# Optimization experiments

Measured on AMD Instinct MI355X. Metric: run time of the kernel, lower is better.

## Reference

```python
import jax, jax.numpy as jnp
import numpy as np

VOCAB, D_IN, D_H, D_OUT = 32000, 512, 1024, 32000
B, S = 64, 512

def setup_inputs() -> dict:
    key = jax.random.key(0)
    ks = jax.random.split(key, 6)
    xav = lambda k, shp: jax.random.uniform(k, shp, jnp.float32, -1.0, 1.0) * np.sqrt(6.0 / (shp[0] + shp[1]))
    return {
        "tokens": jax.random.randint(ks[0], (B, S), 0, VOCAB),
        "h0": jnp.zeros((B, D_H), jnp.float32),
        "embed_table": jax.random.normal(ks[1], (VOCAB, D_IN), jnp.float32),
        "W_ih": xav(ks[2], (D_IN, D_H)),
        "W_hh": xav(ks[3], (D_H, D_H)),
        "bias_hh": jnp.zeros((D_H,), jnp.float32),
        "W_out": xav(ks[4], (D_H, D_OUT)),
        "b_out": jnp.zeros((D_OUT,), jnp.float32),
    }

def reference(tokens, h0, embed_table, W_ih, W_hh, bias_hh, W_out, b_out):
    # embed: [B,S,D_in] -> seq-first [S,B,D_in]
    x = embed_table[tokens].transpose(1, 0, 2)
    # precompute input projection for all timesteps (one big GEMM)
    xw = jnp.einsum("sbi,ih->sbh", x, W_ih) + bias_hh

    def step(h, xw_t):
        h_new = jnp.tanh(xw_t + h @ W_hh)
        return h_new, None

    h_last, _ = jax.lax.scan(step, h0, xw)
    y_pred = h_last @ W_out + b_out  # [B, D_OUT]
    return y_pred
```

## Files before the change

### kernel.cpp

```cpp
#include <hip/hip_runtime.h>

#define D_IN 512
#define D_H 1024
#define D_OUT 32000
#define NB 64
#define NS 512

typedef __attribute__((ext_vector_type(8))) short short8;
typedef __attribute__((ext_vector_type(8))) __bf16 bf16x8;
typedef __attribute__((ext_vector_type(4))) float f32x4;

__device__ __forceinline__ unsigned short f2bf(float f) {
  unsigned int u = __float_as_uint(f);
  u += 0x7fffu + ((u >> 16) & 1u);
  return (unsigned short)(u >> 16);
}
__device__ __forceinline__ float bf2f(unsigned short s) {
  return __uint_as_float(((unsigned int)s) << 16);
}

__device__ __forceinline__ f32x4 mfma_bf16(short8 a, short8 b, f32x4 c) {
  return __builtin_amdgcn_mfma_f32_16x16x32_bf16(
      __builtin_bit_cast(bf16x8, a), __builtin_bit_cast(bf16x8, b), c, 0, 0, 0);
}

union HQ { unsigned long long q[2]; short8 s; };

__global__ __launch_bounds__(256) void rnn_init(const float* __restrict__ h0,
                                                unsigned short* __restrict__ hex,
                                                unsigned int* __restrict__ flags) {
  int idx = blockIdx.x * 256 + threadIdx.x;
  int bg = idx >> 10;
  int k = idx & 1023;
  int g = bg >> 4, bl = bg & 15;
  float v = h0[idx];
  unsigned short hh = f2bf(v);
  unsigned short hl = f2bf(v - bf2f(hh));
  size_t base = ((size_t)(g * 2 + 0) * 2) * 16384 + (size_t)bl * 1024 + k;
  hex[base] = hh;
  hex[base + 16384] = hl;
  if (blockIdx.x == 0) flags[threadIdx.x] = 0u;
}

__global__ __launch_bounds__(256) void rnn_pack_wih(const float* __restrict__ W_ih,
                                                    unsigned short* __restrict__ bhi,
                                                    unsigned short* __restrict__ blo) {
  int idx = blockIdx.x * 256 + threadIdx.x;
  int j = idx & 7;
  int l = (idx >> 3) & 63;
  int kc = (idx >> 9) & 15;
  int nc = idx >> 13;
  int k = kc * 32 + ((l >> 4) << 3) + j;
  int n = nc * 16 + (l & 15);
  float v = W_ih[(size_t)k * D_H + n];
  unsigned short h = f2bf(v);
  bhi[idx] = h;
  blo[idx] = f2bf(v - bf2f(h));
}

__global__ __launch_bounds__(256) void rnn_stage1(const int* __restrict__ tokens,
                                                  const float* __restrict__ embed,
                                                  const unsigned short* __restrict__ bhi,
                                                  const unsigned short* __restrict__ blo,
                                                  const float* __restrict__ bias,
                                                  float* __restrict__ xw) {
  int bx = blockIdx.x;
  int mt = bx >> 4, nt = bx & 15;
  int tid = threadIdx.x;
  int w = tid >> 6, l = tid & 63;
  int q = l >> 4;

  int m = mt * 64 + w * 16 + (l & 15);
  int b = m & 63, t = m >> 6;
  int tok = tokens[b * NS + t];
  const float* arow = embed + (size_t)tok * D_IN;

  f32x4 acc[4];
#pragma unroll
  for (int i = 0; i < 4; ++i) acc[i] = (f32x4){0.f, 0.f, 0.f, 0.f};

  for (int c = 0; c < 16; ++c) {
    const float* ap = arow + c * 32 + q * 8;
    float4 f0 = *(const float4*)ap;
    float4 f1 = *(const float4*)(ap + 4);
    float fa[8] = {f0.x, f0.y, f0.z, f0.w, f1.x, f1.y, f1.z, f1.w};
    short8 ahi, alo;
#pragma unroll
    for (int j = 0; j < 8; ++j) {
      unsigned short hh = f2bf(fa[j]);
      ahi[j] = (short)hh;
      alo[j] = (short)f2bf(fa[j] - bf2f(hh));
    }
#pragma unroll
    for (int ni = 0; ni < 4; ++ni) {
      int ncg = nt * 4 + ni;
      size_t boff = ((size_t)(ncg * 16 + c) * 64 + l) * 8;
      short8 bh = *(const short8*)(bhi + boff);
      short8 bl_ = *(const short8*)(blo + boff);
      acc[ni] = mfma_bf16(ahi, bh, acc[ni]);
      acc[ni] = mfma_bf16(alo, bh, acc[ni]);
      acc[ni] = mfma_bf16(ahi, bl_, acc[ni]);
    }
  }

#pragma unroll
  for (int ni = 0; ni < 4; ++ni) {
    int col = nt * 64 + ni * 16 + (l & 15);
    float bv = bias[col];
#pragma unroll
    for (int r = 0; r < 4; ++r) {
      int row = mt * 64 + w * 16 + q * 4 + r;
      xw[(size_t)row * D_H + col] = acc[ni][r] + bv;
    }
  }
}

__global__ __launch_bounds__(256, 1) void rnn_recur(const float* __restrict__ xw,
                                                    const float* __restrict__ W_hh,
                                                    unsigned short* __restrict__ hex,
                                                    unsigned int* __restrict__ flags,
                                                    float* __restrict__ h_last) {
  __shared__ short Whi[32768];
  __shared__ short Wlo[32768];
  __shared__ float red[4][16][33];

  const int tid = threadIdx.x;
  const int bx = blockIdx.x;
  const int g = bx >> 5;
  const int jt = bx & 31;
  const int jcol0 = jt * 32;
  const int w = tid >> 6;
  const int l = tid & 63;
  const int q = l >> 4;
  const int b_lane = l & 15;

  for (int v = tid; v < 32768; v += 256) {
    int j = v & 7;
    int ll = (v >> 3) & 63;
    int c = (v >> 9) & 31;
    int s = v >> 14;
    int k = c * 32 + ((ll >> 4) << 3) + j;
    int n = s * 16 + (ll & 15);
    float wv = W_hh[(size_t)k * D_H + jcol0 + n];
    unsigned short hh = f2bf(wv);
    Whi[v] = (short)hh;
    Wlo[v] = (short)f2bf(wv - bf2f(hh));
  }
  __syncthreads();

  unsigned int* flg = flags + g * 32;

  const int be = tid >> 4;
  const int je2 = (tid & 15) * 2;
  const int brow = g * 16 + be;

  for (int t = 1; t <= NS; ++t) {
    const float* xwp = xw + ((size_t)(t - 1) * 64 + brow) * D_H + jcol0 + je2;
    float xv0 = xwp[0];
    float xv1 = xwp[1];

    if (tid < 64) {
      unsigned int target = (unsigned int)(t - 1);
      while (1) {
        unsigned int v = __hip_atomic_load(&flg[l & 31], __ATOMIC_RELAXED,
                                           __HIP_MEMORY_SCOPE_AGENT);
        if (__all((int)(v >= target))) break;
      }
    }
    __syncthreads();

    int rbuf = (t - 1) & 1;
    const unsigned long long* hhi =
        (const unsigned long long*)(hex + ((size_t)(g * 2 + rbuf) * 2 + 0) * 16384);
    const unsigned long long* hlo =
        (const unsigned long long*)(hex + ((size_t)(g * 2 + rbuf) * 2 + 1) * 16384);

    HQ ha[8], hl_[8];
#pragma unroll
    for (int i = 0; i < 8; ++i) {
      int c = w * 8 + i;
      int k = c * 32 + q * 8;
      size_t qi = ((size_t)b_lane * 1024 + k) >> 2;
      ha[i].q[0] = __hip_atomic_load(hhi + qi, __ATOMIC_RELAXED, __HIP_MEMORY_SCOPE_AGENT);
      ha[i].q[1] = __hip_atomic_load(hhi + qi + 1, __ATOMIC_RELAXED, __HIP_MEMORY_SCOPE_AGENT);
      hl_[i].q[0] = __hip_atomic_load(hlo + qi, __ATOMIC_RELAXED, __HIP_MEMORY_SCOPE_AGENT);
      hl_[i].q[1] = __hip_atomic_load(hlo + qi + 1, __ATOMIC_RELAXED, __HIP_MEMORY_SCOPE_AGENT);
    }

    f32x4 a00 = {0.f, 0.f, 0.f, 0.f}, a01 = a00, a02 = a00;
    f32x4 a10 = a00, a11 = a00, a12 = a00;
#pragma unroll
    for (int i = 0; i < 8; ++i) {
      int c = w * 8 + i;
      short8 bh0 = *(const short8*)(Whi + c * 512 + l * 8);
      short8 bl0 = *(const short8*)(Wlo + c * 512 + l * 8);
      short8 bh1 = *(const short8*)(Whi + 16384 + c * 512 + l * 8);
      short8 bl1 = *(const short8*)(Wlo + 16384 + c * 512 + l * 8);
      a00 = mfma_bf16(ha[i].s, bh0, a00);
      a01 = mfma_bf16(hl_[i].s, bh0, a01);
      a02 = mfma_bf16(ha[i].s, bl0, a02);
      a10 = mfma_bf16(ha[i].s, bh1, a10);
      a11 = mfma_bf16(hl_[i].s, bh1, a11);
      a12 = mfma_bf16(ha[i].s, bl1, a12);
    }
    f32x4 s0 = a00 + a01 + a02;
    f32x4 s1 = a10 + a11 + a12;
#pragma unroll
    for (int r = 0; r < 4; ++r) {
      red[w][q * 4 + r][b_lane] = s0[r];
      red[w][q * 4 + r][16 + b_lane] = s1[r];
    }
    __syncthreads();

    float z0 = red[0][be][je2] + red[1][be][je2] + red[2][be][je2] +
               red[3][be][je2] + xv0;
    float z1 = red[0][be][je2 + 1] + red[1][be][je2 + 1] + red[2][be][je2 + 1] +
               red[3][be][je2 + 1] + xv1;
    float hv0 = tanhf(z0);
    float hv1 = tanhf(z1);
    unsigned short h0h = f2bf(hv0), h1h = f2bf(hv1);
    unsigned short h0l = f2bf(hv0 - bf2f(h0h)), h1l = f2bf(hv1 - bf2f(h1h));
    int wbuf = t & 1;
    size_t obase = (size_t)be * 1024 + jcol0 + je2;
    unsigned int* dhi =
        (unsigned int*)(hex + ((size_t)(g * 2 + wbuf) * 2 + 0) * 16384 + obase);
    unsigned int* dlo =
        (unsigned int*)(hex + ((size_t)(g * 2 + wbuf) * 2 + 1) * 16384 + obase);
    unsigned int phi = (unsigned int)h0h | ((unsigned int)h1h << 16);
    unsigned int plo = (unsigned int)h0l | ((unsigned int)h1l << 16);
    __hip_atomic_store(dhi, phi, __ATOMIC_RELAXED, __HIP_MEMORY_SCOPE_AGENT);
    __hip_atomic_store(dlo, plo, __ATOMIC_RELAXED, __HIP_MEMORY_SCOPE_AGENT);
    if (t == NS) {
      h_last[(size_t)brow * 1024 + jcol0 + je2] = hv0;
      h_last[(size_t)brow * 1024 + jcol0 + je2 + 1] = hv1;
    }

    asm volatile("s_waitcnt vmcnt(0)" ::: "memory");
    __syncthreads();
    if (tid == 0)
      __hip_atomic_store(&flg[jt], (unsigned int)t, __ATOMIC_RELAXED,
                         __HIP_MEMORY_SCOPE_AGENT);
  }
}

__global__ __launch_bounds__(256, 2) void rnn_out(const float* __restrict__ h_last,
                                                  const float* __restrict__ W_out,
                                                  const float* __restrict__ b_out,
                                                  float* __restrict__ out) {
  __shared__ float smem[16384];
  int tid = threadIdx.x;
  int jl = tid & 127;
  int kh = tid >> 7;
  int j = blockIdx.x * 128 + jl;

  float acc[64];
#pragma unroll
  for (int b = 0; b < 64; ++b) acc[b] = 0.f;

  for (int kc = 0; kc < 4; ++kc) {
    __syncthreads();
    for (int v = tid; v < 16384; v += 256) {
      int kh2 = v >> 13;
      int b = (v >> 7) & 63;
      int kk = v & 127;
      smem[v] = h_last[(size_t)b * 1024 + kh2 * 512 + kc * 128 + kk];
    }
    __syncthreads();
    int kbase = kh * 512 + kc * 128;
    for (int kkc = 0; kkc < 16; ++kkc) {
      float wreg[8];
#pragma unroll
      for (int i = 0; i < 8; ++i)
        wreg[i] = W_out[(size_t)(kbase + kkc * 8 + i) * D_OUT + j];
#pragma unroll
      for (int b = 0; b < 64; ++b) {
        const float* hp = &smem[kh * 8192 + b * 128 + kkc * 8];
#pragma unroll
        for (int i = 0; i < 8; ++i) acc[b] += hp[i] * wreg[i];
      }
    }
  }
  __syncthreads();
  if (kh == 1) {
#pragma unroll
    for (int b = 0; b < 64; ++b) smem[jl * 65 + b] = acc[b];
  }
  __syncthreads();
  if (kh == 0) {
    float bo = b_out[j];
#pragma unroll
    for (int b = 0; b < 64; ++b)
      out[(size_t)b * D_OUT + j] = acc[b] + smem[jl * 65 + b] + bo;
  }
}

extern "C" void kernel_launch(void* const* d_in, const int* in_sizes, int n_in,
                              void* d_out, int out_size, void* d_ws, size_t ws_size,
                              hipStream_t stream) {
  const int* tokens = (const int*)d_in[0];
  const float* h0 = (const float*)d_in[1];
  const float* embed = (const float*)d_in[2];
  const float* W_ih = (const float*)d_in[3];
  const float* W_hh = (const float*)d_in[4];
  const float* bias_hh = (const float*)d_in[5];
  const float* W_out = (const float*)d_in[6];
  const float* b_out = (const float*)d_in[7];
  float* out = (float*)d_out;

  char* ws = (char*)d_ws;
  float* xw = (float*)(ws);
  unsigned short* wih_hi = (unsigned short*)(ws + 134217728);
  unsigned short* wih_lo = (unsigned short*)(ws + 135266304);
  unsigned short* hex = (unsigned short*)(ws + 136314880);
  unsigned int* flags = (unsigned int*)(ws + 136839168);
  float* h_last = (float*)(ws + 136840192);

  rnn_init<<<256, 256, 0, stream>>>(h0, hex, flags);
  rnn_pack_wih<<<2048, 256, 0, stream>>>(W_ih, wih_hi, wih_lo);
  rnn_stage1<<<8192, 256, 0, stream>>>(tokens, embed, wih_hi, wih_lo, bias_hh, xw);
  rnn_recur<<<128, 256, 0, stream>>>(xw, W_hh, hex, flags, h_last);
  rnn_out<<<250, 256, 0, stream>>>(h_last, W_out, b_out, out);
}
```

Measured before the change: 3.600 ms.

## Replace flag barrier with tagged hidden-state words for flagless cross-block sync

Removes the per-step flag array and its store-wait-barrier-flag handshake in the recurrent kernel. Each hidden-state element pair is now packed as a 64-bit word (hi and lo bf16 parts) with a parity tag in the low bit of the lo parts. Readers spin on the data itself until every tag matches the expected phase. This also drops a __syncthreads per step, using a double-buffered reduction scratch instead. In exchange it loses one mantissa bit of the lo correction term and relies on 64-bit atomic loads and stores being single-copy atomic.

```diff
diff --git a/kernel.cpp b/kernel.cpp
--- a/kernel.cpp
+++ b/kernel.cpp
@@ -24,22 +24,22 @@
       __builtin_bit_cast(bf16x8, a), __builtin_bit_cast(bf16x8, b), c, 0, 0, 0);
 }
 
-union HQ { unsigned long long q[2]; short8 s; };
-
 __global__ __launch_bounds__(256) void rnn_init(const float* __restrict__ h0,
-                                                unsigned short* __restrict__ hex,
-                                                unsigned int* __restrict__ flags) {
+                                                unsigned long long* __restrict__ hx) {
   int idx = blockIdx.x * 256 + threadIdx.x;
-  int bg = idx >> 10;
-  int k = idx & 1023;
+  int bg = idx >> 9;
+  int k2 = idx & 511;
   int g = bg >> 4, bl = bg & 15;
-  float v = h0[idx];
-  unsigned short hh = f2bf(v);
-  unsigned short hl = f2bf(v - bf2f(hh));
-  size_t base = ((size_t)(g * 2 + 0) * 2) * 16384 + (size_t)bl * 1024 + k;
-  hex[base] = hh;
-  hex[base + 16384] = hl;
-  if (blockIdx.x == 0) flags[threadIdx.x] = 0u;
+  float v0 = h0[bg * 1024 + k2 * 2];
+  float v1 = h0[bg * 1024 + k2 * 2 + 1];
+  unsigned int h0h = f2bf(v0), h1h = f2bf(v1);
+  unsigned int l0 = (unsigned int)f2bf(v0 - bf2f((unsigned short)h0h)) & ~1u;
+  unsigned int l1 = (unsigned int)f2bf(v1 - bf2f((unsigned short)h1h)) & ~1u;
+  unsigned long long real =
+      (unsigned long long)(h0h | (h1h << 16)) |
+      ((unsigned long long)(l0 | (l1 << 16)) << 32);
+  hx[((size_t)(g * 2 + 0) * 16 + bl) * 512 + k2] = real;
+  hx[((size_t)(g * 2 + 1) * 16 + bl) * 512 + k2] = 0x0001000100000000ull;
 }
 
 __global__ __launch_bounds__(256) void rnn_pack_wih(const float* __restrict__ W_ih,
@@ -117,12 +117,11 @@
 
 __global__ __launch_bounds__(256, 1) void rnn_recur(const float* __restrict__ xw,
                                                     const float* __restrict__ W_hh,
-                                                    unsigned short* __restrict__ hex,
-                                                    unsigned int* __restrict__ flags,
+                                                    unsigned long long* __restrict__ hx,
                                                     float* __restrict__ h_last) {
   __shared__ short Whi[32768];
   __shared__ short Wlo[32768];
-  __shared__ float red[4][16][33];
+  __shared__ float red[2][4][16][33];
 
   const int tid = threadIdx.x;
   const int bx = blockIdx.x;
@@ -148,98 +147,92 @@
   }
   __syncthreads();
 
-  unsigned int* flg = flags + g * 32;
-
   const int be = tid >> 4;
   const int je2 = (tid & 15) * 2;
   const int brow = g * 16 + be;
 
   for (int t = 1; t <= NS; ++t) {
+    const int rbuf = (t - 1) & 1;
+    const int wbuf = t & 1;
+    const unsigned int etagp = (((t - 1) >> 1) & 1) ? 0x00010001u : 0u;
+    const unsigned int wtag = (unsigned int)((t >> 1) & 1);
+
     const float* xwp = xw + ((size_t)(t - 1) * 64 + brow) * D_H + jcol0 + je2;
     float xv0 = xwp[0];
     float xv1 = xwp[1];
 
-    if (tid < 64) {
-      unsigned int target = (unsigned int)(t - 1);
-      while (1) {
-        unsigned int v = __hip_atomic_load(&flg[l & 31], __ATOMIC_RELAXED,
-                                           __HIP_MEMORY_SCOPE_AGENT);
-        if (__all((int)(v >= target))) break;
+    const unsigned long long* hp =
+        hx + ((size_t)(g * 2 + rbuf) * 16 + b_lane) * 512;
+    unsigned long long hb[32];
+    while (1) {
+#pragma unroll
+      for (int i = 0; i < 8; ++i) {
+        int u0 = (w * 8 + i) * 16 + q * 4;
+#pragma unroll
+        for (int j = 0; j < 4; ++j)
+          hb[i * 4 + j] = __hip_atomic_load(hp + u0 + j, __ATOMIC_RELAXED,
+                                            __HIP_MEMORY_SCOPE_AGENT);
       }
-    }
-    __syncthreads();
-
-    int rbuf = (t - 1) & 1;
-    const unsigned long long* hhi =
-        (const unsigned long long*)(hex + ((size_t)(g * 2 + rbuf) * 2 + 0) * 16384);
-    const unsigned long long* hlo =
-        (const unsigned long long*)(hex + ((size_t)(g * 2 + rbuf) * 2 + 1) * 16384);
-
-    HQ ha[8], hl_[8];
+      unsigned int bad = 0;
+#pragma unroll
+      for (int m = 0; m < 32; ++m)
+        bad |= ((unsigned int)(hb[m] >> 32) ^ etagp) & 0x00010001u;
+      if (__all(bad == 0)) break;
+      __builtin_amdgcn_s_sleep(1);
+    }
+
+    f32x4 a00 = {0.f, 0.f, 0.f, 0.f}, a01 = a00, a02 = a00;
+    f32x4 a10 = a00, a11 = a00, a12 = a00;
 #pragma unroll
     for (int i = 0; i < 8; ++i) {
       int c = w * 8 + i;
-      int k = c * 32 + q * 8;
-      size_t qi = ((size_t)b_lane * 1024 + k) >> 2;
-      ha[i].q[0] = __hip_atomic_load(hhi + qi, __ATOMIC_RELAXED, __HIP_MEMORY_SCOPE_AGENT);
-      ha[i].q[1] = __hip_atomic_load(hhi + qi + 1, __ATOMIC_RELAXED, __HIP_MEMORY_SCOPE_AGENT);
-      hl_[i].q[0] = __hip_atomic_load(hlo + qi, __ATOMIC_RELAXED, __HIP_MEMORY_SCOPE_AGENT);
-      hl_[i].q[1] = __hip_atomic_load(hlo + qi + 1, __ATOMIC_RELAXED, __HIP_MEMORY_SCOPE_AGENT);
-    }
-
-    f32x4 a00 = {0.f, 0.f, 0.f, 0.f}, a01 = a00, a02 = a00;
-    f32x4 a10 = a00, a11 = a00, a12 = a00;
-#pragma unroll
-    for (int i = 0; i < 8; ++i) {
-      int c = w * 8 + i;
+      uint4 ah = {(unsigned int)hb[i * 4 + 0], (unsigned int)hb[i * 4 + 1],
+                  (unsigned int)hb[i * 4 + 2], (unsigned int)hb[i * 4 + 3]};
+      uint4 al = {(unsigned int)(hb[i * 4 + 0] >> 32),
+                  (unsigned int)(hb[i * 4 + 1] >> 32),
+                  (unsigned int)(hb[i * 4 + 2] >> 32),
+                  (unsigned int)(hb[i * 4 + 3] >> 32)};
+      short8 as = __builtin_bit_cast(short8, ah);
+      short8 ls = __builtin_bit_cast(short8, al);
       short8 bh0 = *(const short8*)(Whi + c * 512 + l * 8);
       short8 bl0 = *(const short8*)(Wlo + c * 512 + l * 8);
       short8 bh1 = *(const short8*)(Whi + 16384 + c * 512 + l * 8);
       short8 bl1 = *(const short8*)(Wlo + 16384 + c * 512 + l * 8);
-      a00 = mfma_bf16(ha[i].s, bh0, a00);
-      a01 = mfma_bf16(hl_[i].s, bh0, a01);
-      a02 = mfma_bf16(ha[i].s, bl0, a02);
-      a10 = mfma_bf16(ha[i].s, bh1, a10);
-      a11 = mfma_bf16(hl_[i].s, bh1, a11);
-      a12 = mfma_bf16(ha[i].s, bl1, a12);
+      a00 = mfma_bf16(as, bh0, a00);
+      a01 = mfma_bf16(ls, bh0, a01);
+      a02 = mfma_bf16(as, bl0, a02);
+      a10 = mfma_bf16(as, bh1, a10);
+      a11 = mfma_bf16(ls, bh1, a11);
+      a12 = mfma_bf16(as, bl1, a12);
     }
     f32x4 s0 = a00 + a01 + a02;
     f32x4 s1 = a10 + a11 + a12;
 #pragma unroll
     for (int r = 0; r < 4; ++r) {
-      red[w][q * 4 + r][b_lane] = s0[r];
-      red[w][q * 4 + r][16 + b_lane] = s1[r];
+      red[rbuf][w][q * 4 + r][b_lane] = s0[r];
+      red[rbuf][w][q * 4 + r][16 + b_lane] = s1[r];
     }
     __syncthreads();
 
-    float z0 = red[0][be][je2] + red[1][be][je2] + red[2][be][je2] +
-               red[3][be][je2] + xv0;
-    float z1 = red[0][be][je2 + 1] + red[1][be][je2 + 1] + red[2][be][je2 + 1] +
-               red[3][be][je2 + 1] + xv1;
+    float z0 = red[rbuf][0][be][je2] + red[rbuf][1][be][je2] +
+               red[rbuf][2][be][je2] + red[rbuf][3][be][je2] + xv0;
+    float z1 = red[rbuf][0][be][je2 + 1] + red[rbuf][1][be][je2 + 1] +
+               red[rbuf][2][be][je2 + 1] + red[rbuf][3][be][je2 + 1] + xv1;
     float hv0 = tanhf(z0);
     float hv1 = tanhf(z1);
-    unsigned short h0h = f2bf(hv0), h1h = f2bf(hv1);
-    unsigned short h0l = f2bf(hv0 - bf2f(h0h)), h1l = f2bf(hv1 - bf2f(h1h));
-    int wbuf = t & 1;
-    size_t obase = (size_t)be * 1024 + jcol0 + je2;
-    unsigned int* dhi =
-        (unsigned int*)(hex + ((size_t)(g * 2 + wbuf) * 2 + 0) * 16384 + obase);
-    unsigned int* dlo =
-        (unsigned int*)(hex + ((size_t)(g * 2 + wbuf) * 2 + 1) * 16384 + obase);
-    unsigned int phi = (unsigned int)h0h | ((unsigned int)h1h << 16);
-    unsigned int plo = (unsigned int)h0l | ((unsigned int)h1l << 16);
-    __hip_atomic_store(dhi, phi, __ATOMIC_RELAXED, __HIP_MEMORY_SCOPE_AGENT);
-    __hip_atomic_store(dlo, plo, __ATOMIC_RELAXED, __HIP_MEMORY_SCOPE_AGENT);
+    unsigned int h0h = f2bf(hv0), h1h = f2bf(hv1);
+    unsigned int l0 = ((unsigned int)f2bf(hv0 - bf2f((unsigned short)h0h)) & ~1u) | wtag;
+    unsigned int l1 = ((unsigned int)f2bf(hv1 - bf2f((unsigned short)h1h)) & ~1u) | wtag;
+    unsigned long long val =
+        (unsigned long long)(h0h | (h1h << 16)) |
+        ((unsigned long long)(l0 | (l1 << 16)) << 32);
+    unsigned long long* dst =
+        hx + ((size_t)(g * 2 + wbuf) * 16 + be) * 512 + ((jcol0 + je2) >> 1);
+    __hip_atomic_store(dst, val, __ATOMIC_RELAXED, __HIP_MEMORY_SCOPE_AGENT);
     if (t == NS) {
       h_last[(size_t)brow * 1024 + jcol0 + je2] = hv0;
       h_last[(size_t)brow * 1024 + jcol0 + je2 + 1] = hv1;
     }
-
-    asm volatile("s_waitcnt vmcnt(0)" ::: "memory");
-    __syncthreads();
-    if (tid == 0)
-      __hip_atomic_store(&flg[jt], (unsigned int)t, __ATOMIC_RELAXED,
-                         __HIP_MEMORY_SCOPE_AGENT);
   }
 }
 
@@ -311,13 +304,12 @@
   float* xw = (float*)(ws);
   unsigned short* wih_hi = (unsigned short*)(ws + 134217728);
   unsigned short* wih_lo = (unsigned short*)(ws + 135266304);
-  unsigned short* hex = (unsigned short*)(ws + 136314880);
-  unsigned int* flags = (unsigned int*)(ws + 136839168);
-  float* h_last = (float*)(ws + 136840192);
-
-  rnn_init<<<256, 256, 0, stream>>>(h0, hex, flags);
+  unsigned long long* hx = (unsigned long long*)(ws + 136314880);
+  float* h_last = (float*)(ws + 136839168);
+
+  rnn_init<<<128, 256, 0, stream>>>(h0, hx);
   rnn_pack_wih<<<2048, 256, 0, stream>>>(W_ih, wih_hi, wih_lo);
   rnn_stage1<<<8192, 256, 0, stream>>>(tokens, embed, wih_hi, wih_lo, bias_hh, xw);
-  rnn_recur<<<128, 256, 0, stream>>>(xw, W_hh, hex, flags, h_last);
+  rnn_recur<<<128, 256, 0, stream>>>(xw, W_hh, hx, h_last);
   rnn_out<<<250, 256, 0, stream>>>(h_last, W_out, b_out, out);
 }
```

Result: slower. 4.155 ms (+15.4%).
